# Kernel optimization log

Measured on AMD Instinct MI355X. Metric: run time of the kernel, lower is better.

## Reference

```python
import jax, jax.numpy as jnp
import numpy as np

V, D, H, L, E, DH, K, PMAX = 50257, 128, 4, 4, 8, 512, 2, 256
B, T = 8, 256


def setup_inputs() -> dict:
    key = jax.random.key(0)
    ks = jax.random.split(key, 10)
    s = 0.02
    def n(k, shape):
        return jax.random.normal(k, shape, jnp.float32) * s
    return dict(
        idx=jax.random.randint(ks[0], (B, T), 0, V),
        tok_emb=n(ks[1], (V, D)),
        pos_emb=n(ks[2], (PMAX, D)),
        ln1_g=jnp.ones((L, D), jnp.float32), ln1_b=jnp.zeros((L, D), jnp.float32),
        in_w=n(ks[3], (L, 3 * D, D)), in_b=jnp.zeros((L, 3 * D), jnp.float32),
        out_w=n(ks[4], (L, D, D)), out_b=jnp.zeros((L, D), jnp.float32),
        ln2_g=jnp.ones((L, D), jnp.float32), ln2_b=jnp.zeros((L, D), jnp.float32),
        gate_w=n(ks[5], (L, E, D)),
        w1=n(ks[6], (L, E, DH, D)),
        w2=n(ks[7], (L, E, D, DH)),
        lnf_g=jnp.ones((D,), jnp.float32), lnf_b=jnp.zeros((D,), jnp.float32),
        lm_w=n(ks[8], (V, D)),
    )


def _ln(x, g, b):
    mu = x.mean(-1, keepdims=True)
    var = jnp.var(x, -1, keepdims=True)
    return (x - mu) / jnp.sqrt(var + 1e-5) * g + b


def _moe(x, gw, w1, w2):
    # x: [N, D]; top-2 sparse MoE, computed densely per expert then combined.
    logits = x @ gw.T                              # [N, E]
    probs = jax.nn.softmax(logits, -1)
    topw, topi = jax.lax.top_k(probs, K)           # [N, K]
    topw = topw / topw.sum(-1, keepdims=True)
    we = (topw[..., None] * jax.nn.one_hot(topi, E, dtype=x.dtype)).sum(1)  # [N, E]
    h = jax.nn.silu(jnp.einsum('nd,ehd->neh', x, w1))   # [N, E, DH]
    y = jnp.einsum('neh,edh->ned', h, w2)               # [N, E, D]
    return jnp.einsum('ned,ne->nd', y, we)


def reference(idx, tok_emb, pos_emb, ln1_g, ln1_b, in_w, in_b, out_w, out_b,
              ln2_g, ln2_b, gate_w, w1, w2, lnf_g, lnf_b, lm_w):
    b, t = idx.shape
    x = tok_emb[idx] + pos_emb[:t]                 # [B, T, D]
    dh = D // H
    scale = 1.0 / np.sqrt(dh)
    for l in range(L):
        xl = _ln(x, ln1_g[l], ln1_b[l])
        qkv = xl @ in_w[l].T + in_b[l]
        q, k, v = jnp.split(qkv, 3, -1)
        q = q.reshape(b, t, H, dh)
        k = k.reshape(b, t, H, dh)
        v = v.reshape(b, t, H, dh)
        att = jax.nn.softmax(jnp.einsum('bqhd,bkhd->bhqk', q, k) * scale, -1)
        o = jnp.einsum('bhqk,bkhd->bqhd', att, v).reshape(b, t, D)
        x = x + o @ out_w[l].T + out_b[l]
        x2 = _ln(x, ln2_g[l], ln2_b[l]).reshape(b * t, D)
        x = x + _moe(x2, gate_w[l], w1[l], w2[l]).reshape(b, t, D)
    return _ln(x, lnf_g, lnf_b) @ lm_w.T           # [B, T, V]
```

## Files before the change

### kernel.cpp

```cpp
#include <hip/hip_runtime.h>
#include <math.h>

#define NTOK 2048
#define DD   128
#define NHEAD 4
#define DHEAD 32
#define NLAYER 4
#define NEXP 8
#define DHID 512
#define NVOCAB 50257
#define VPAD  50304
#define SEQ   256
#define NBATCH 8

typedef __attribute__((ext_vector_type(8))) short short8v;
typedef __attribute__((ext_vector_type(4))) float f32x4;

__device__ __forceinline__ unsigned short nm_bf16r(float f) {
  unsigned u = __float_as_uint(f);
  u += 0x7fffu + ((u >> 16) & 1u);
  return (unsigned short)(u >> 16);
}

__device__ __forceinline__ float nm_silu(float a) {
  return a / (1.f + __expf(-a));
}

template<int N4>
__device__ __forceinline__ float nm_dotv(const float* __restrict__ a,
                                         const float* __restrict__ w) {
  const float4* a4 = (const float4*)a;
  const float4* w4 = (const float4*)w;
  float sx = 0.f, sy = 0.f, sz = 0.f, sw = 0.f;
#pragma unroll 16
  for (int k = 0; k < N4; ++k) {
    float4 av = a4[k], wv = w4[k];
    sx = fmaf(av.x, wv.x, sx);
    sy = fmaf(av.y, wv.y, sy);
    sz = fmaf(av.z, wv.z, sz);
    sw = fmaf(av.w, wv.w, sw);
  }
  return (sx + sy) + (sz + sw);
}

#define C3_LMW 6438912ull
#define C3_W1  6963200ull
#define C3_ALL 7487488ull
#define CVTB   7312
__global__ __launch_bounds__(256) void nm_init(
    const int* __restrict__ idx, const float* __restrict__ tok,
    const float* __restrict__ pos, const float* __restrict__ g,
    const float* __restrict__ b, const float* __restrict__ lmw,
    const float* __restrict__ w1l3, const float* __restrict__ w2l3,
    float* __restrict__ x, float* __restrict__ xl,
    unsigned short* __restrict__ lmwb, unsigned short* __restrict__ w1b3,
    unsigned short* __restrict__ w2b3, int* __restrict__ zp) {
  int bid = blockIdx.x, tid = threadIdx.x;
  if (bid < CVTB) {
    size_t base = ((size_t)bid * 256 + tid) * 4;
    if (base < (size_t)NVOCAB * DD) {
      float4 v = *(const float4*)(lmw + base);
      ushort4 us = {nm_bf16r(v.x), nm_bf16r(v.y), nm_bf16r(v.z), nm_bf16r(v.w)};
      *(ushort4*)(lmwb + base) = us;
    } else if (base < C3_LMW) {
      ushort4 us = {0, 0, 0, 0};
      *(ushort4*)(lmwb + base) = us;
    } else if (base < C3_W1) {
      size_t j = base - C3_LMW;
      float4 v = *(const float4*)(w1l3 + j);
      ushort4 us = {nm_bf16r(v.x), nm_bf16r(v.y), nm_bf16r(v.z), nm_bf16r(v.w)};
      *(ushort4*)(w1b3 + j) = us;
    } else {
      size_t j = base - C3_W1;
      float4 v = *(const float4*)(w2l3 + j);
      ushort4 us = {nm_bf16r(v.x), nm_bf16r(v.y), nm_bf16r(v.z), nm_bf16r(v.w)};
      *(ushort4*)(w2b3 + j) = us;
    }
  } else if (bid < CVTB + NTOK / 4) {
    int n = (bid - CVTB) * 4 + (tid >> 6);
    int lane = tid & 63;
    int t = idx[n];
    float v0 = tok[(size_t)t * DD + lane]      + pos[(n % SEQ) * DD + lane];
    float v1 = tok[(size_t)t * DD + lane + 64] + pos[(n % SEQ) * DD + lane + 64];
    x[n * DD + lane]      = v0;
    x[n * DD + lane + 64] = v1;
    float s = v0 + v1;
#pragma unroll
    for (int o = 32; o > 0; o >>= 1) s += __shfl_xor(s, o, 64);
    float mu = s * (1.f / 128.f);
    float d0 = v0 - mu, d1 = v1 - mu;
    float q = d0 * d0 + d1 * d1;
#pragma unroll
    for (int o = 32; o > 0; o >>= 1) q += __shfl_xor(q, o, 64);
    float rstd = rsqrtf(q * (1.f / 128.f) + 1e-5f);
    xl[n * DD + lane]      = d0 * rstd * g[lane]      + b[lane];
    xl[n * DD + lane + 64] = d1 * rstd * g[lane + 64] + b[lane + 64];
  } else {
    if (tid < 68) zp[tid] = 0;
  }
}

__global__ void nm_embed_ln(const int* __restrict__ idx, const float* __restrict__ tok,
                            const float* __restrict__ pos, const float* __restrict__ g,
                            const float* __restrict__ b, float* __restrict__ x,
                            float* __restrict__ xlf) {
  int n = blockIdx.x, lane = threadIdx.x;
  int t = idx[n];
  float v0 = tok[(size_t)t * DD + lane]      + pos[(n % SEQ) * DD + lane];
  float v1 = tok[(size_t)t * DD + lane + 64] + pos[(n % SEQ) * DD + lane + 64];
  x[n * DD + lane]      = v0;
  x[n * DD + lane + 64] = v1;
  float s = v0 + v1;
#pragma unroll
  for (int o = 32; o > 0; o >>= 1) s += __shfl_xor(s, o, 64);
  float mu = s * (1.f / 128.f);
  float d0 = v0 - mu, d1 = v1 - mu;
  float q = d0 * d0 + d1 * d1;
#pragma unroll
  for (int o = 32; o > 0; o >>= 1) q += __shfl_xor(q, o, 64);
  float rstd = rsqrtf(q * (1.f / 128.f) + 1e-5f);
  xlf[n * DD + lane]      = d0 * rstd * g[lane]      + b[lane];
  xlf[n * DD + lane + 64] = d1 * rstd * g[lane + 64] + b[lane + 64];
}

__global__ void nm_ln(const float* __restrict__ in, const float* __restrict__ g,
                      const float* __restrict__ b, float* __restrict__ out) {
  int n = blockIdx.x, lane = threadIdx.x;
  float v0 = in[n * DD + lane], v1 = in[n * DD + lane + 64];
  float s = v0 + v1;
#pragma unroll
  for (int o = 32; o > 0; o >>= 1) s += __shfl_xor(s, o, 64);
  float mu = s * (1.f / 128.f);
  float d0 = v0 - mu, d1 = v1 - mu;
  float q = d0 * d0 + d1 * d1;
#pragma unroll
  for (int o = 32; o > 0; o >>= 1) q += __shfl_xor(q, o, 64);
  float rstd = rsqrtf(q * (1.f / 128.f) + 1e-5f);
  out[n * DD + lane]      = d0 * rstd * g[lane]      + b[lane];
  out[n * DD + lane + 64] = d1 * rstd * g[lane + 64] + b[lane + 64];
}

__global__ void nm_combine_ln(const float* __restrict__ yb, const int* __restrict__ posm,
                              const float* __restrict__ topw, float* __restrict__ x,
                              const float* __restrict__ g, const float* __restrict__ b,
                              float* __restrict__ xl, unsigned short* __restrict__ xb) {
  int n = blockIdx.x, lane = threadIdx.x;
  float w0 = topw[2 * n], w1 = topw[2 * n + 1];
  int p0 = posm[2 * n], p1 = posm[2 * n + 1];
  float v0 = x[n * DD + lane]      + w0 * yb[(size_t)p0 * DD + lane]
                                   + w1 * yb[(size_t)p1 * DD + lane];
  float v1 = x[n * DD + lane + 64] + w0 * yb[(size_t)p0 * DD + lane + 64]
                                   + w1 * yb[(size_t)p1 * DD + lane + 64];
  x[n * DD + lane]      = v0;
  x[n * DD + lane + 64] = v1;
  float s = v0 + v1;
#pragma unroll
  for (int o = 32; o > 0; o >>= 1) s += __shfl_xor(s, o, 64);
  float mu = s * (1.f / 128.f);
  float d0 = v0 - mu, d1 = v1 - mu;
  float q = d0 * d0 + d1 * d1;
#pragma unroll
  for (int o = 32; o > 0; o >>= 1) q += __shfl_xor(q, o, 64);
  float rstd = rsqrtf(q * (1.f / 128.f) + 1e-5f);
  float o0 = d0 * rstd * g[lane]      + b[lane];
  float o1 = d1 * rstd * g[lane + 64] + b[lane + 64];
  xl[n * DD + lane]      = o0;
  xl[n * DD + lane + 64] = o1;
  if (xb) {
    xb[n * DD + lane]      = nm_bf16r(o0);
    xb[n * DD + lane + 64] = nm_bf16r(o1);
  }
}

template<int F, int MT>
__global__ __launch_bounds__(256) void nm_gemm2(
    const float* __restrict__ A, const float* __restrict__ B,
    float* __restrict__ C, const float* __restrict__ bias,
    int M, int N, int K,
    const int* __restrict__ list, const int* __restrict__ cnt,
    const int* __restrict__ off) {
  constexpr bool GA = F & 1, SI = F & 2, BI = F & 4, GR = F & 16;
  constexpr int RG = MT / 64;
  __shared__ __align__(16) float As[64][MT + 4];
  __shared__ __align__(16) float Bs[64][68];
  int tid = threadIdx.x;
  int n0 = blockIdx.x * 64, m0 = blockIdx.y * MT;
  int Mloc = M, o = 0;
  const float* Bb = B;
  if constexpr (GR) {
    int e = blockIdx.z;
    Mloc = cnt[e];
    if (m0 >= Mloc) return;
    o = off[e];
    Bb = B + (size_t)e * (size_t)N * K;
  }
  int tm = tid & 15, tn = tid >> 4;
  float acc[RG * 4][4] = {};
  for (int kc = 0; kc < K; kc += 64) {
#pragma unroll
    for (int i = 0; i < RG * 4; ++i) {
      int f = tid + 256 * i;
      int r = f >> 4, c4 = f & 15;
      int mi = m0 + r;
      if (mi >= Mloc) mi = m0;
      const float* ar;
      if constexpr (GA) ar = A + (size_t)(list[o + mi] >> 1) * K;
      else              ar = A + (size_t)(o + mi) * K;
      float4 v = *(const float4*)(ar + kc + c4 * 4);
      int k = c4 * 4;
      As[k][r] = v.x; As[k + 1][r] = v.y; As[k + 2][r] = v.z; As[k + 3][r] = v.w;
    }
#pragma unroll
    for (int i = 0; i < 4; ++i) {
      int f = tid + 256 * i;
      int r = f >> 4, c4 = f & 15;
      const float* br = Bb + (size_t)(n0 + r) * K + kc + c4 * 4;
      float4 v = *(const float4*)br;
      int k = c4 * 4;
      Bs[k][r] = v.x; Bs[k + 1][r] = v.y; Bs[k + 2][r] = v.z; Bs[k + 3][r] = v.w;
    }
    __syncthreads();
#pragma unroll 16
    for (int k = 0; k < 64; ++k) {
      float4 b = *(const float4*)&Bs[k][tn * 4];
#pragma unroll
      for (int g2 = 0; g2 < RG; ++g2) {
        float4 a = *(const float4*)&As[k][g2 * 64 + tm * 4];
        acc[g2*4+0][0] = fmaf(a.x, b.x, acc[g2*4+0][0]);
        acc[g2*4+0][1] = fmaf(a.x, b.y, acc[g2*4+0][1]);
        acc[g2*4+0][2] = fmaf(a.x, b.z, acc[g2*4+0][2]);
        acc[g2*4+0][3] = fmaf(a.x, b.w, acc[g2*4+0][3]);
        acc[g2*4+1][0] = fmaf(a.y, b.x, acc[g2*4+1][0]);
        acc[g2*4+1][1] = fmaf(a.y, b.y, acc[g2*4+1][1]);
        acc[g2*4+1][2] = fmaf(a.y, b.z, acc[g2*4+1][2]);
        acc[g2*4+1][3] = fmaf(a.y, b.w, acc[g2*4+1][3]);
        acc[g2*4+2][0] = fmaf(a.z, b.x, acc[g2*4+2][0]);
        acc[g2*4+2][1] = fmaf(a.z, b.y, acc[g2*4+2][1]);
        acc[g2*4+2][2] = fmaf(a.z, b.z, acc[g2*4+2][2]);
        acc[g2*4+2][3] = fmaf(a.z, b.w, acc[g2*4+2][3]);
        acc[g2*4+3][0] = fmaf(a.w, b.x, acc[g2*4+3][0]);
        acc[g2*4+3][1] = fmaf(a.w, b.y, acc[g2*4+3][1]);
        acc[g2*4+3][2] = fmaf(a.w, b.z, acc[g2*4+3][2]);
        acc[g2*4+3][3] = fmaf(a.w, b.w, acc[g2*4+3][3]);
      }
    }
    __syncthreads();
  }
  float4 bv = {0.f, 0.f, 0.f, 0.f};
  if constexpr (BI) bv = *(const float4*)(bias + n0 + tn * 4);
#pragma unroll
  for (int g2 = 0; g2 < RG; ++g2) {
#pragma unroll
    for (int i = 0; i < 4; ++i) {
      int row = m0 + g2 * 64 + tm * 4 + i;
      if (GR && row >= Mloc) continue;
      float* cr = C + (size_t)(o + row) * N + n0 + tn * 4;
      float r0 = acc[g2 * 4 + i][0], r1 = acc[g2 * 4 + i][1];
      float r2 = acc[g2 * 4 + i][2], r3 = acc[g2 * 4 + i][3];
      if constexpr (BI) { r0 += bv.x; r1 += bv.y; r2 += bv.z; r3 += bv.w; }
      if constexpr (SI) { r0 = nm_silu(r0); r1 = nm_silu(r1); r2 = nm_silu(r2); r3 = nm_silu(r3); }
      float4 st = {r0, r1, r2, r3};
      *(float4*)cr = st;
    }
  }
}

template<int F, int KK>
__global__ __launch_bounds__(256) void nm_bgemm(
    const unsigned short* __restrict__ A, const unsigned short* __restrict__ B,
    float* __restrict__ Cf, unsigned short* __restrict__ Cb,
    const float* __restrict__ bias, int M, int N,
    const int* __restrict__ list, const int* __restrict__ cnt,
    const int* __restrict__ off) {
  constexpr bool GA = F & 1, SI = F & 2, BI = F & 4, SB = F & 8, GR = F & 16;
  int wave = threadIdx.x >> 6, lane = threadIdx.x & 63;
  int n0 = blockIdx.x * 32;
  int m0 = blockIdx.y * 128 + wave * 32;
  int Mloc = M, o = 0;
  const unsigned short* Bb = B;
  if constexpr (GR) {
    int e = blockIdx.z;
    Mloc = cnt[e];
    o = off[e];
    Bb = B + (size_t)e * (size_t)N * KK;
  }
  if (m0 >= Mloc) return;
  int lr = lane & 15, lk = (lane >> 4) * 8;
  const unsigned short* arow[2];
#pragma unroll
  for (int i = 0; i < 2; ++i) {
    int mi = m0 + i * 16 + lr;
    if (mi >= Mloc) mi = Mloc - 1;
    int r = GA ? (list[o + mi] >> 1) : (o + mi);
    arow[i] = A + (size_t)r * KK;
  }
  const unsigned short* brow[2] = { Bb + (size_t)(n0 + lr) * KK,
                                    Bb + (size_t)(n0 + 16 + lr) * KK };
  f32x4 acc[2][2] = {};
#pragma unroll
  for (int ks = 0; ks < KK / 32; ++ks) {
    int kb = ks * 32 + lk;
    short8v a0 = *(const short8v*)(arow[0] + kb);
    short8v a1 = *(const short8v*)(arow[1] + kb);
    short8v b0 = *(const short8v*)(brow[0] + kb);
    short8v b1 = *(const short8v*)(brow[1] + kb);
    acc[0][0] = __builtin_amdgcn_mfma_f32_16x16x32_bf16(a0, b0, acc[0][0], 0, 0, 0);
    acc[0][1] = __builtin_amdgcn_mfma_f32_16x16x32_bf16(a0, b1, acc[0][1], 0, 0, 0);
    acc[1][0] = __builtin_amdgcn_mfma_f32_16x16x32_bf16(a1, b0, acc[1][0], 0, 0, 0);
    acc[1][1] = __builtin_amdgcn_mfma_f32_16x16x32_bf16(a1, b1, acc[1][1], 0, 0, 0);
  }
  float bc[2] = {0.f, 0.f};
  if constexpr (BI) {
    bc[0] = bias[n0 + (lane & 15)];
    bc[1] = bias[n0 + 16 + (lane & 15)];
  }
#pragma unroll
  for (int i = 0; i < 2; ++i) {
    int rbase = m0 + i * 16 + (lane >> 4) * 4;
#pragma unroll
    for (int r = 0; r < 4; ++r) {
      int row = rbase + r;
      if (GR && row >= Mloc) continue;
#pragma unroll
      for (int j = 0; j < 2; ++j) {
        float v = acc[i][j][r];
        if constexpr (BI) v += bc[j];
        if constexpr (SI) v = nm_silu(v);
        int col = n0 + j * 16 + (lane & 15);
        if constexpr (SB) Cb[(size_t)(o + row) * N + col] = nm_bf16r(v);
        else              Cf[(size_t)(o + row) * N + col] = v;
      }
    }
  }
}

__global__ __launch_bounds__(256) void nm_oplng(
    const float* __restrict__ ao, const float* __restrict__ w,
    const float* __restrict__ bias, float* __restrict__ x,
    const float* __restrict__ g, const float* __restrict__ b,
    float* __restrict__ xlf, unsigned short* __restrict__ xlb,
    const float* __restrict__ gw,
    int* __restrict__ topi, float* __restrict__ topw, int* __restrict__ cnt,
    int* __restrict__ ticket, int* __restrict__ off, int* __restrict__ list,
    int* __restrict__ posm) {
  __shared__ __align__(16) float As[64][36];
  __shared__ __align__(16) float Bs[64][132];
  __shared__ float Ls[32][9];
  __shared__ int doR;
  __shared__ int cv[NEXP], lcur[NEXP];
  int tid = threadIdx.x;
  int m0 = blockIdx.x * 32;
  int tm = tid >> 5, tn = tid & 31;
  float acc[4][4] = {};
  for (int kc = 0; kc < DD; kc += 64) {
#pragma unroll
    for (int i = 0; i < 2; ++i) {
      int ch = tid + 256 * i, r = ch >> 4, c4 = ch & 15;
      float4 v = *(const float4*)(ao + (size_t)(m0 + r) * DD + kc + c4 * 4);
      int k = c4 * 4;
      As[k][r] = v.x; As[k + 1][r] = v.y; As[k + 2][r] = v.z; As[k + 3][r] = v.w;
    }
#pragma unroll
    for (int i = 0; i < 8; ++i) {
      int ch = tid + 256 * i, r = ch >> 4, c4 = ch & 15;
      float4 v = *(const float4*)(w + (size_t)r * DD + kc + c4 * 4);
      int k = c4 * 4;
      Bs[k][r] = v.x; Bs[k + 1][r] = v.y; Bs[k + 2][r] = v.z; Bs[k + 3][r] = v.w;
    }
    __syncthreads();
#pragma unroll 8
    for (int k = 0; k < 64; ++k) {
      float4 a = *(const float4*)&As[k][tm * 4];
      float4 bb = *(const float4*)&Bs[k][tn * 4];
      acc[0][0] = fmaf(a.x, bb.x, acc[0][0]); acc[0][1] = fmaf(a.x, bb.y, acc[0][1]);
      acc[0][2] = fmaf(a.x, bb.z, acc[0][2]); acc[0][3] = fmaf(a.x, bb.w, acc[0][3]);
      acc[1][0] = fmaf(a.y, bb.x, acc[1][0]); acc[1][1] = fmaf(a.y, bb.y, acc[1][1]);
      acc[1][2] = fmaf(a.y, bb.z, acc[1][2]); acc[1][3] = fmaf(a.y, bb.w, acc[1][3]);
      acc[2][0] = fmaf(a.z, bb.x, acc[2][0]); acc[2][1] = fmaf(a.z, bb.y, acc[2][1]);
      acc[2][2] = fmaf(a.z, bb.z, acc[2][2]); acc[2][3] = fmaf(a.z, bb.w, acc[2][3]);
      acc[3][0] = fmaf(a.w, bb.x, acc[3][0]); acc[3][1] = fmaf(a.w, bb.y, acc[3][1]);
      acc[3][2] = fmaf(a.w, bb.z, acc[3][2]); acc[3][3] = fmaf(a.w, bb.w, acc[3][3]);
    }
    __syncthreads();
  }
  float4 bv = *(const float4*)(bias + tn * 4);
  float rr[4][4], s1[4], s2[4];
#pragma unroll
  for (int i = 0; i < 4; ++i) {
    int rw = m0 + tm * 4 + i;
    float4 xv = *(const float4*)(x + (size_t)rw * DD + tn * 4);
    float r0 = acc[i][0] + bv.x + xv.x;
    float r1 = acc[i][1] + bv.y + xv.y;
    float r2 = acc[i][2] + bv.z + xv.z;
    float r3 = acc[i][3] + bv.w + xv.w;
    rr[i][0] = r0; rr[i][1] = r1; rr[i][2] = r2; rr[i][3] = r3;
    float4 st = {r0, r1, r2, r3};
    *(float4*)(x + (size_t)rw * DD + tn * 4) = st;
    s1[i] = r0 + r1 + r2 + r3;
    s2[i] = r0 * r0 + r1 * r1 + r2 * r2 + r3 * r3;
  }
#pragma unroll
  for (int o = 16; o >= 1; o >>= 1) {
#pragma unroll
    for (int i = 0; i < 4; ++i) {
      s1[i] += __shfl_xor(s1[i], o, 64);
      s2[i] += __shfl_xor(s2[i], o, 64);
    }
  }
  float4 gv  = *(const float4*)(g + tn * 4);
  float4 bbv = *(const float4*)(b + tn * 4);
#pragma unroll
  for (int i = 0; i < 4; ++i) {
    int rw = m0 + tm * 4 + i;
    float mu = s1[i] * (1.f / 128.f);
    float var = s2[i] * (1.f / 128.f) - mu * mu;
    float rstd = rsqrtf(var + 1e-5f);
    float y0 = (rr[i][0] - mu) * rstd * gv.x + bbv.x;
    float y1 = (rr[i][1] - mu) * rstd * gv.y + bbv.y;
    float y2 = (rr[i][2] - mu) * rstd * gv.z + bbv.z;
    float y3 = (rr[i][3] - mu) * rstd * gv.w + bbv.w;
    float4 yv = {y0, y1, y2, y3};
    if (xlf) *(float4*)(xlf + (size_t)rw * DD + tn * 4) = yv;
    if (xlb) {
      ushort4 us = {nm_bf16r(y0), nm_bf16r(y1), nm_bf16r(y2), nm_bf16r(y3)};
      *(ushort4*)(xlb + (size_t)rw * DD + tn * 4) = us;
    }
    *(float4*)&Bs[tm * 4 + i][tn * 4] = yv;
  }
  __syncthreads();
  int grow = tid >> 3, ge = tid & 7;
  const float4* xr = (const float4*)&Bs[grow][0];
  const float4* wr = (const float4*)(gw + (size_t)ge * DD);
  float sx = 0.f, sy = 0.f, sz = 0.f, sw = 0.f;
#pragma unroll
  for (int k2 = 0; k2 < 32; ++k2) {
    float4 a = xr[k2], w4 = wr[k2];
    sx = fmaf(a.x, w4.x, sx); sy = fmaf(a.y, w4.y, sy);
    sz = fmaf(a.z, w4.z, sz); sw = fmaf(a.w, w4.w, sw);
  }
  Ls[grow][ge] = (sx + sy) + (sz + sw);
  __syncthreads();
  if (ge == 0) {
    float gl[NEXP];
#pragma unroll
    for (int e = 0; e < NEXP; ++e) gl[e] = Ls[grow][e];
    int i0 = 0;
#pragma unroll
    for (int e = 1; e < NEXP; ++e) if (gl[e] > gl[i0]) i0 = e;
    int i1 = (i0 == 0) ? 1 : 0;
#pragma unroll
    for (int e = 0; e < NEXP; ++e) { if (e != i0 && gl[e] > gl[i1]) i1 = e; }
    float p1 = __expf(gl[i1] - gl[i0]);
    float inv = 1.f / (1.f + p1);
    int n = m0 + grow;
    topi[2 * n] = i0; topi[2 * n + 1] = i1;
    topw[2 * n] = inv; topw[2 * n + 1] = p1 * inv;
    atomicAdd(cnt + i0, 1);
    atomicAdd(cnt + i1, 1);
  }
  __syncthreads();
  if (tid == 0) {
    __threadfence();
    doR = (atomicAdd(ticket, 1) == 63);
    if (doR) __threadfence();
  }
  __syncthreads();
  if (doR) {
    if (tid < NEXP) cv[tid] = atomicAdd(cnt + tid, 0);
    __syncthreads();
    if (tid < NEXP) {
      int o2 = 0;
      for (int e = 0; e < tid; ++e) o2 += cv[e];
      lcur[tid] = o2;
      off[tid] = o2;
    }
    __syncthreads();
    for (int t = tid; t < 2 * NTOK; t += 256) {
      int e = topi[t];
      int p = atomicAdd(&lcur[e], 1);
      list[p] = t;
      posm[t] = p;
    }
  }
}

__global__ __launch_bounds__(256) void nm_attn2(const float* __restrict__ qkv,
                                                float* __restrict__ o) {
  __shared__ __align__(16) float Ks[SEQ][DHEAD];
  __shared__ __align__(16) float Vs[SEQ][DHEAD];
  __shared__ float mbuf[32][9], sbuf[32][9];
  __shared__ __align__(16) float accbuf[32][36];
  int bh = blockIdx.x;
  int b = bh >> 2, h = bh & 3;
  int qt = blockIdx.y;
  int tid = threadIdx.x;
  const float* base = qkv + (size_t)b * SEQ * 384;
  for (int f = tid; f < SEQ * 8; f += 256) {
    int t = f >> 3, c4 = f & 7;
    float4 kv = *(const float4*)(base + (size_t)t * 384 + 128 + h * DHEAD + c4 * 4);
    float4 vv = *(const float4*)(base + (size_t)t * 384 + 256 + h * DHEAD + c4 * 4);
    *(float4*)&Ks[t][c4 * 4] = kv;
    *(float4*)&Vs[t][c4 * 4] = vv;
  }
  __syncthreads();
  int q = tid & 31, slot = tid >> 5;
  int tq = qt * 32 + q;
  float qv[DHEAD];
  const float4* q4 = (const float4*)(base + (size_t)tq * 384 + h * DHEAD);
#pragma unroll
  for (int k = 0; k < 8; ++k) {
    float4 v = q4[k];
    qv[4*k] = v.x; qv[4*k+1] = v.y; qv[4*k+2] = v.z; qv[4*k+3] = v.w;
  }
  float m = -1e30f, s = 0.f, acc[DHEAD];
#pragma unroll
  for (int d = 0; d < DHEAD; ++d) acc[d] = 0.f;
  const float scale = 0.17677669529663687f;
  int j0 = slot * 32;
  for (int jj = 0; jj < 32; ++jj) {
    int j = j0 + jj;
    const float4* kr = (const float4*)Ks[j];
    float sc = 0.f;
#pragma unroll
    for (int k = 0; k < 8; ++k) {
      float4 v = kr[k];
      sc += qv[4*k]*v.x + qv[4*k+1]*v.y + qv[4*k+2]*v.z + qv[4*k+3]*v.w;
    }
    sc *= scale;
    float mn = fmaxf(m, sc);
    float f = __expf(m - mn), p = __expf(sc - mn);
    s = s * f + p;
    const float4* vr = (const float4*)Vs[j];
#pragma unroll
    for (int k = 0; k < 8; ++k) {
      float4 v = vr[k];
      acc[4*k]   = acc[4*k]  * f + p * v.x;
      acc[4*k+1] = acc[4*k+1]* f + p * v.y;
      acc[4*k+2] = acc[4*k+2]* f + p * v.z;
      acc[4*k+3] = acc[4*k+3]* f + p * v.w;
    }
    m = mn;
  }
  mbuf[q][slot] = m;
  sbuf[q][slot] = s;
  __syncthreads();
  float M = mbuf[q][0];
#pragma unroll
  for (int t = 1; t < 8; ++t) M = fmaxf(M, mbuf[q][t]);
  float S = 0.f;
#pragma unroll
  for (int t = 0; t < 8; ++t) S += sbuf[q][t] * __expf(mbuf[q][t] - M);
  float w = __expf(m - M);
#pragma unroll
  for (int d = 0; d < DHEAD; ++d) acc[d] *= w;
#pragma unroll
  for (int p = 0; p < 8; ++p) {
    if (slot == p) {
      if (p == 0) {
#pragma unroll
        for (int d = 0; d < DHEAD; ++d) accbuf[q][d] = acc[d];
      } else {
#pragma unroll
        for (int d = 0; d < DHEAD; ++d) accbuf[q][d] += acc[d];
      }
    }
    __syncthreads();
  }
  if (slot == 0) sbuf[q][8] = 1.f / S;
  __syncthreads();
  int q2 = tid >> 3, c4 = tid & 7;
  float inv = sbuf[q2][8];
  float4 v = *(const float4*)&accbuf[q2][c4 * 4];
  v.x *= inv; v.y *= inv; v.z *= inv; v.w *= inv;
  *(float4*)(o + (size_t)(b * SEQ + qt * 32 + q2) * DD + h * DHEAD + c4 * 4) = v;
}

__global__ void nm_qkv(const float* __restrict__ xl, const float* __restrict__ w,
                       const float* __restrict__ bias, float* __restrict__ qkv) {
  __shared__ __align__(16) float xs[DD];
  int n = blockIdx.x, tid = threadIdx.x;
  xs[tid] = xl[n * DD + tid];
  __syncthreads();
#pragma unroll
  for (int jj = 0; jj < 3; ++jj) {
    int j = tid + jj * 128;
    qkv[(size_t)n * 384 + j] = nm_dotv<32>(xs, w + (size_t)j * DD) + bias[j];
  }
}

__global__ void nm_outproj(const float* __restrict__ ao, const float* __restrict__ w,
                           const float* __restrict__ bias, float* __restrict__ x) {
  __shared__ __align__(16) float os[DD];
  int n = blockIdx.x, tid = threadIdx.x;
  os[tid] = ao[n * DD + tid];
  __syncthreads();
  x[n * DD + tid] += nm_dotv<32>(os, w + (size_t)tid * DD) + bias[tid];
}

__global__ void nm_moe(const float* __restrict__ x2, const float* __restrict__ gw,
                       const float* __restrict__ w1, const float* __restrict__ w2,
                       float* __restrict__ x) {
  __shared__ __align__(16) float xs[DD];
  __shared__ __align__(16) float hs[DHID];
  __shared__ float gl[NEXP];
  __shared__ int   ei[2];
  __shared__ float ew[2];
  int n = blockIdx.x, tid = threadIdx.x;
  if (tid < DD) xs[tid] = x2[n * DD + tid];
  __syncthreads();
  if (tid < NEXP) gl[tid] = nm_dotv<32>(xs, gw + (size_t)tid * DD);
  __syncthreads();
  if (tid == 0) {
    int i0 = 0;
#pragma unroll
    for (int e = 1; e < NEXP; ++e) if (gl[e] > gl[i0]) i0 = e;
    int i1 = (i0 == 0) ? 1 : 0;
    for (int e = 0; e < NEXP; ++e) { if (e == i0) continue; if (gl[e] > gl[i1]) i1 = e; }
    float p1 = __expf(gl[i1] - gl[i0]);
    float inv = 1.f / (1.f + p1);
    ei[0] = i0; ei[1] = i1; ew[0] = inv; ew[1] = p1 * inv;
  }
  __syncthreads();
  float yacc = 0.f;
  for (int t2 = 0; t2 < 2; ++t2) {
    int e = ei[t2];
    float wt = ew[t2];
    const float* w1e = w1 + (size_t)e * DHID * DD;
#pragma unroll
    for (int jj = 0; jj < 2; ++jj) {
      int j = tid + jj * 256;
      float a = nm_dotv<32>(xs, w1e + (size_t)j * DD);
      hs[j] = nm_silu(a);
    }
    __syncthreads();
    if (tid < DD) yacc += wt * nm_dotv<128>(hs, w2 + ((size_t)e * DD + tid) * DHID);
    __syncthreads();
  }
  if (tid < DD) x[n * DD + tid] += yacc;
}

__device__ __forceinline__ short8v nm_cvt8(const float* p) {
  const float4* p4 = (const float4*)p;
  float4 a = p4[0], b = p4[1];
  short8v r;
  r[0] = (short)nm_bf16r(a.x); r[1] = (short)nm_bf16r(a.y);
  r[2] = (short)nm_bf16r(a.z); r[3] = (short)nm_bf16r(a.w);
  r[4] = (short)nm_bf16r(b.x); r[5] = (short)nm_bf16r(b.y);
  r[6] = (short)nm_bf16r(b.z); r[7] = (short)nm_bf16r(b.w);
  return r;
}

__global__ __launch_bounds__(256) void nm_lmhead_f32(
    const float* __restrict__ xf, const float* __restrict__ lmw,
    float* __restrict__ out) {
  int wave = threadIdx.x >> 6, lane = threadIdx.x & 63;
  int wr = wave >> 1, wc = wave & 1;
  int row0 = blockIdx.y * 128 + wr * 64;
  int col0 = blockIdx.x * 128 + wc * 64;
  int lr = lane & 15, lk = (lane >> 4) * 8;
  f32x4 acc[4][4] = {};
#pragma unroll
  for (int ks = 0; ks < 4; ++ks) {
    int kb = ks * 32 + lk;
    short8v a[4], b[4];
#pragma unroll
    for (int i = 0; i < 4; ++i)
      a[i] = nm_cvt8(xf + (size_t)(row0 + i * 16 + lr) * DD + kb);
#pragma unroll
    for (int j = 0; j < 4; ++j) {
      int c = col0 + j * 16 + lr;
      if (c < NVOCAB) b[j] = nm_cvt8(lmw + (size_t)c * DD + kb);
      else {
        short8v z;
#pragma unroll
        for (int e = 0; e < 8; ++e) z[e] = 0;
        b[j] = z;
      }
    }
#pragma unroll
    for (int i = 0; i < 4; ++i)
#pragma unroll
      for (int j = 0; j < 4; ++j)
        acc[i][j] = __builtin_amdgcn_mfma_f32_16x16x32_bf16(a[i], b[j], acc[i][j], 0, 0, 0);
  }
  int cr = (lane >> 4) * 4;
#pragma unroll
  for (int j = 0; j < 4; ++j) {
    int c = col0 + j * 16 + (lane & 15);
    if (c < NVOCAB) {
#pragma unroll
      for (int i = 0; i < 4; ++i)
#pragma unroll
        for (int r = 0; r < 4; ++r)
          out[(size_t)(row0 + i * 16 + cr + r) * NVOCAB + c] = acc[i][j][r];
    }
  }
}

__global__ __launch_bounds__(256) void nm_lmhead2(
    const unsigned short* __restrict__ xfb, const unsigned short* __restrict__ lmwb,
    float* __restrict__ out) {
  __shared__ __align__(16) unsigned char smem[132 * 128 * 4];
  unsigned short* Ab = (unsigned short*)smem;
  unsigned short* Bb = Ab + 128 * 128;
  int tid = threadIdx.x;
  int row0 = blockIdx.y * 128, col0 = blockIdx.x * 128;
#pragma unroll
  for (int i = 0; i < 8; ++i) {
    int ch = tid + i * 256;
    int r = ch >> 4, s = ch & 15;
    int sg = s ^ (r & 7);
    *(short8v*)&Ab[r * 128 + s * 8] =
        *(const short8v*)(xfb + (size_t)(row0 + r) * DD + sg * 8);
    *(short8v*)&Bb[r * 128 + s * 8] =
        *(const short8v*)(lmwb + (size_t)(col0 + r) * DD + sg * 8);
  }
  __syncthreads();
  int wave = tid >> 6, lane = tid & 63;
  int wr = wave >> 1, wc = wave & 1;
  int lr = lane & 15, hk = lane >> 4;
  f32x4 acc[4][4] = {};
#pragma unroll
  for (int ks = 0; ks < 4; ++ks) {
    int sg = ks * 4 + hk;
    int sx = (sg ^ (lr & 7)) * 8;
    short8v a[4], b[4];
#pragma unroll
    for (int i = 0; i < 4; ++i)
      a[i] = *(const short8v*)&Ab[(wr * 64 + i * 16 + lr) * 128 + sx];
#pragma unroll
    for (int j = 0; j < 4; ++j)
      b[j] = *(const short8v*)&Bb[(wc * 64 + j * 16 + lr) * 128 + sx];
#pragma unroll
    for (int i = 0; i < 4; ++i)
#pragma unroll
      for (int j = 0; j < 4; ++j)
        acc[i][j] = __builtin_amdgcn_mfma_f32_16x16x32_bf16(a[i], b[j], acc[i][j], 0, 0, 0);
  }
  __syncthreads();
  float* Cs = (float*)smem;
  int hi4 = hk * 4;
#pragma unroll
  for (int j = 0; j < 4; ++j)
#pragma unroll
    for (int i = 0; i < 4; ++i)
#pragma unroll
      for (int r = 0; r < 4; ++r)
        Cs[(wr * 64 + i * 16 + hi4 + r) * 132 + wc * 64 + j * 16 + lr] = acc[i][j][r];
  __syncthreads();
  bool full = (col0 + 128 <= NVOCAB);
#pragma unroll 4
  for (int rr = 0; rr < 32; ++rr) {
    int row = wave * 32 + rr;
    float v0 = Cs[row * 132 + lane];
    float v1 = Cs[row * 132 + 64 + lane];
    size_t base = (size_t)(row0 + row) * NVOCAB + col0;
    if (full) {
      out[base + lane] = v0;
      out[base + 64 + lane] = v1;
    } else {
      if (col0 + lane < NVOCAB)      out[base + lane] = v0;
      if (col0 + 64 + lane < NVOCAB) out[base + 64 + lane] = v1;
    }
  }
}

extern "C" void kernel_launch(void* const* d_in, const int* in_sizes, int n_in,
                              void* d_out, int out_size, void* d_ws, size_t ws_size,
                              hipStream_t stream) {
  const int*   idx   = (const int*)  d_in[0];
  const float* tok   = (const float*)d_in[1];
  const float* pos   = (const float*)d_in[2];
  const float* ln1g  = (const float*)d_in[3];
  const float* ln1b  = (const float*)d_in[4];
  const float* inw   = (const float*)d_in[5];
  const float* inb   = (const float*)d_in[6];
  const float* outw  = (const float*)d_in[7];
  const float* outb  = (const float*)d_in[8];
  const float* ln2g  = (const float*)d_in[9];
  const float* ln2b  = (const float*)d_in[10];
  const float* gatew = (const float*)d_in[11];
  const float* w1    = (const float*)d_in[12];
  const float* w2    = (const float*)d_in[13];
  const float* lnfg  = (const float*)d_in[14];
  const float* lnfb  = (const float*)d_in[15];
  const float* lmw   = (const float*)d_in[16];
  float* out = (float*)d_out;

  float* ws   = (float*)d_ws;
  float* x    = ws;
  float* xl   = x    + NTOK * DD;
  float* qkv  = xl   + NTOK * DD;
  float* ao   = qkv  + NTOK * 384;
  float* topw = ao   + NTOK * DD;
  float* H    = topw + 2 * NTOK;
  float* yb   = H    + 2 * NTOK * DHID;
  int*   topi = (int*)(yb + 2 * NTOK * DD);
  int*   list = topi + 2 * NTOK;
  int*   posm = list + 2 * NTOK;
  int*   cnt  = posm + 2 * NTOK;
  int*   offs = cnt  + NLAYER * NEXP;
  int*   tick = offs + NLAYER * NEXP;
  unsigned short* xlb  = (unsigned short*)(tick + 8);
  unsigned short* Hb   = xlb + NTOK * DD;
  unsigned short* xfb  = Hb  + 2 * NTOK * DHID;
  unsigned short* w1b3 = xfb + NTOK * DD;
  unsigned short* w2b3 = w1b3 + NEXP * DHID * DD;
  unsigned short* lmwb = w2b3 + NEXP * DD * DHID;
  const size_t need = (size_t)((char*)(lmwb + (size_t)VPAD * DD) - (char*)d_ws);
  const bool pre = (ws_size >= need);

  const float* w1l3 = w1 + (size_t)3 * NEXP * DHID * DD;
  const float* w2l3 = w2 + (size_t)3 * NEXP * DD * DHID;

  if (pre) {
    nm_init<<<CVTB + NTOK / 4 + 1, 256, 0, stream>>>(
        idx, tok, pos, ln1g, ln1b, lmw, w1l3, w2l3, x, xl, lmwb, w1b3, w2b3, cnt);
    for (int l = 0; l < NLAYER; ++l) {
      nm_gemm2<4, 128><<<dim3(384 / 64, NTOK / 128), 256, 0, stream>>>(
          xl, inw + (size_t)l * 384 * DD, qkv, inb + (size_t)l * 384,
          NTOK, 384, DD, nullptr, nullptr, nullptr);
      nm_attn2<<<dim3(NBATCH * NHEAD, SEQ / 32), 256, 0, stream>>>(qkv, ao);
      nm_oplng<<<NTOK / 32, 256, 0, stream>>>(
          ao, outw + (size_t)l * DD * DD, outb + (size_t)l * DD, x,
          ln2g + l * DD, ln2b + l * DD, xl, (l == 3) ? xlb : (unsigned short*)nullptr,
          gatew + (size_t)l * NEXP * DD, topi, topw, cnt + l * NEXP,
          tick + l, offs + l * NEXP, list, posm);
      int* cnt_l = cnt + l * NEXP;
      int* off_l = offs + l * NEXP;
      if (l < 3) {
        const float* w1l = w1 + (size_t)l * NEXP * DHID * DD;
        const float* w2l = w2 + (size_t)l * NEXP * DD * DHID;
        nm_gemm2<19, 128><<<dim3(DHID / 64, 2 * NTOK / 128, NEXP), 256, 0, stream>>>(
            xl, w1l, H, nullptr, 0, DHID, DD, list, cnt_l, off_l);
        nm_gemm2<16, 64><<<dim3(DD / 64, 2 * NTOK / 64, NEXP), 256, 0, stream>>>(
            H, w2l, yb, nullptr, 0, DD, DHID, nullptr, cnt_l, off_l);
      } else {
        nm_bgemm<27, 128><<<dim3(DHID / 32, 32, NEXP), 256, 0, stream>>>(
            xlb, w1b3, nullptr, Hb, nullptr, 0, DHID, list, cnt_l, off_l);
        nm_bgemm<16, 512><<<dim3(DD / 32, 32, NEXP), 256, 0, stream>>>(
            Hb, w2b3, yb, nullptr, nullptr, 0, DD, nullptr, cnt_l, off_l);
      }
      const float* gN = (l < NLAYER - 1) ? ln1g + (l + 1) * DD : lnfg;
      const float* bN = (l < NLAYER - 1) ? ln1b + (l + 1) * DD : lnfb;
      nm_combine_ln<<<NTOK, 64, 0, stream>>>(
          yb, posm, topw, x, gN, bN, xl,
          (l == NLAYER - 1) ? xfb : (unsigned short*)nullptr);
    }
    nm_lmhead2<<<dim3(VPAD / 128, NTOK / 128), 256, 0, stream>>>(xfb, lmwb, out);
  } else {
    nm_embed_ln<<<NTOK, 64, 0, stream>>>(idx, tok, pos, ln1g, ln1b, x, xl);
    for (int l = 0; l < NLAYER; ++l) {
      nm_qkv<<<NTOK, 128, 0, stream>>>(xl, inw + (size_t)l * 384 * DD,
                                       inb + (size_t)l * 384, qkv);
      nm_attn2<<<dim3(NBATCH * NHEAD, SEQ / 32), 256, 0, stream>>>(qkv, ao);
      nm_outproj<<<NTOK, 128, 0, stream>>>(ao, outw + (size_t)l * DD * DD,
                                           outb + (size_t)l * DD, x);
      nm_ln<<<NTOK, 64, 0, stream>>>(x, ln2g + l * DD, ln2b + l * DD, xl);
      nm_moe<<<NTOK, 256, 0, stream>>>(xl, gatew + (size_t)l * NEXP * DD,
                                       w1 + (size_t)l * NEXP * DHID * DD,
                                       w2 + (size_t)l * NEXP * DD * DHID, x);
      const float* gN = (l < NLAYER - 1) ? ln1g + (l + 1) * DD : lnfg;
      const float* bN = (l < NLAYER - 1) ? ln1b + (l + 1) * DD : lnfb;
      nm_ln<<<NTOK, 64, 0, stream>>>(x, gN, bN, xl);
    }
    nm_lmhead_f32<<<dim3(VPAD / 128, NTOK / 128), 256, 0, stream>>>(xl, lmw, out);
  }
}
```

Baseline: 828.4 us.

## Restructure attention to 16 queries per block with swizzled shared K/V

Replaces the attention kernel with a version that processes 16 queries per block, each split across 16 key slots, stores K/V in shared memory with an XOR-style rotation to avoid bank conflicts, and merges partial softmax states in one pass instead of a serialized 8-step accumulation with repeated barriers. The grid doubles along the query dimension, which increases parallelism at the cost of reloading K/V twice as often. QKV and first MoE GEMM tile heights are also halved to launch more blocks, and the oplng kernel now always writes the fp32 LN output.

```diff
diff --git a/kernel.cpp b/kernel.cpp
--- a/kernel.cpp
+++ b/kernel.cpp
@@ -96,7 +96,7 @@
     xl[n * DD + lane]      = d0 * rstd * g[lane]      + b[lane];
     xl[n * DD + lane + 64] = d1 * rstd * g[lane + 64] + b[lane + 64];
   } else {
-    if (tid < 68) zp[tid] = 0;
+    if (tid < 72) zp[tid] = 0;
   }
 }
 
@@ -338,7 +338,7 @@
     const float* __restrict__ ao, const float* __restrict__ w,
     const float* __restrict__ bias, float* __restrict__ x,
     const float* __restrict__ g, const float* __restrict__ b,
-    float* __restrict__ xlf, unsigned short* __restrict__ xlb,
+    float* __restrict__ xl, unsigned short* __restrict__ xlb,
     const float* __restrict__ gw,
     int* __restrict__ topi, float* __restrict__ topw, int* __restrict__ cnt,
     int* __restrict__ ticket, int* __restrict__ off, int* __restrict__ list,
@@ -420,7 +420,7 @@
     float y2 = (rr[i][2] - mu) * rstd * gv.z + bbv.z;
     float y3 = (rr[i][3] - mu) * rstd * gv.w + bbv.w;
     float4 yv = {y0, y1, y2, y3};
-    if (xlf) *(float4*)(xlf + (size_t)rw * DD + tn * 4) = yv;
+    *(float4*)(xl + (size_t)rw * DD + tn * 4) = yv;
     if (xlb) {
       ushort4 us = {nm_bf16r(y0), nm_bf16r(y1), nm_bf16r(y2), nm_bf16r(y3)};
       *(ushort4*)(xlb + (size_t)rw * DD + tn * 4) = us;
@@ -484,12 +484,11 @@
   }
 }
 
-__global__ __launch_bounds__(256) void nm_attn2(const float* __restrict__ qkv,
+__global__ __launch_bounds__(256) void nm_attn3(const float* __restrict__ qkv,
                                                 float* __restrict__ o) {
-  __shared__ __align__(16) float Ks[SEQ][DHEAD];
-  __shared__ __align__(16) float Vs[SEQ][DHEAD];
-  __shared__ float mbuf[32][9], sbuf[32][9];
-  __shared__ __align__(16) float accbuf[32][36];
+  __shared__ __align__(16) float smem[2 * SEQ * DHEAD];
+  float4* K4 = (float4*)smem;
+  float4* V4 = (float4*)(smem + SEQ * DHEAD);
   int bh = blockIdx.x;
   int b = bh >> 2, h = bh & 3;
   int qt = blockIdx.y;
@@ -497,14 +496,13 @@
   const float* base = qkv + (size_t)b * SEQ * 384;
   for (int f = tid; f < SEQ * 8; f += 256) {
     int t = f >> 3, c4 = f & 7;
-    float4 kv = *(const float4*)(base + (size_t)t * 384 + 128 + h * DHEAD + c4 * 4);
-    float4 vv = *(const float4*)(base + (size_t)t * 384 + 256 + h * DHEAD + c4 * 4);
-    *(float4*)&Ks[t][c4 * 4] = kv;
-    *(float4*)&Vs[t][c4 * 4] = vv;
-  }
-  __syncthreads();
-  int q = tid & 31, slot = tid >> 5;
-  int tq = qt * 32 + q;
+    int pc = (c4 + (t >> 4)) & 7;
+    K4[t * 8 + pc] = *(const float4*)(base + (size_t)t * 384 + 128 + h * DHEAD + c4 * 4);
+    V4[t * 8 + pc] = *(const float4*)(base + (size_t)t * 384 + 256 + h * DHEAD + c4 * 4);
+  }
+  __syncthreads();
+  int qi = tid >> 4, slot = tid & 15;
+  int tq = qt * 16 + qi;
   float qv[DHEAD];
   const float4* q4 = (const float4*)(base + (size_t)tq * 384 + h * DHEAD);
 #pragma unroll
@@ -516,24 +514,22 @@
 #pragma unroll
   for (int d = 0; d < DHEAD; ++d) acc[d] = 0.f;
   const float scale = 0.17677669529663687f;
-  int j0 = slot * 32;
-  for (int jj = 0; jj < 32; ++jj) {
-    int j = j0 + jj;
-    const float4* kr = (const float4*)Ks[j];
+  int sw = slot & 7;
+  for (int jj = 0; jj < 16; ++jj) {
+    int j = slot * 16 + jj;
     float sc = 0.f;
 #pragma unroll
     for (int k = 0; k < 8; ++k) {
-      float4 v = kr[k];
+      float4 v = K4[j * 8 + ((k + sw) & 7)];
       sc += qv[4*k]*v.x + qv[4*k+1]*v.y + qv[4*k+2]*v.z + qv[4*k+3]*v.w;
     }
     sc *= scale;
     float mn = fmaxf(m, sc);
     float f = __expf(m - mn), p = __expf(sc - mn);
     s = s * f + p;
-    const float4* vr = (const float4*)Vs[j];
 #pragma unroll
     for (int k = 0; k < 8; ++k) {
-      float4 v = vr[k];
+      float4 v = V4[j * 8 + ((k + sw) & 7)];
       acc[4*k]   = acc[4*k]  * f + p * v.x;
       acc[4*k+1] = acc[4*k+1]* f + p * v.y;
       acc[4*k+2] = acc[4*k+2]* f + p * v.z;
@@ -541,38 +537,31 @@
     }
     m = mn;
   }
-  mbuf[q][slot] = m;
-  sbuf[q][slot] = s;
-  __syncthreads();
-  float M = mbuf[q][0];
-#pragma unroll
-  for (int t = 1; t < 8; ++t) M = fmaxf(M, mbuf[q][t]);
-  float S = 0.f;
-#pragma unroll
-  for (int t = 0; t < 8; ++t) S += sbuf[q][t] * __expf(mbuf[q][t] - M);
-  float w = __expf(m - M);
-#pragma unroll
-  for (int d = 0; d < DHEAD; ++d) acc[d] *= w;
-#pragma unroll
-  for (int p = 0; p < 8; ++p) {
-    if (slot == p) {
-      if (p == 0) {
-#pragma unroll
-        for (int d = 0; d < DHEAD; ++d) accbuf[q][d] = acc[d];
-      } else {
-#pragma unroll
-        for (int d = 0; d < DHEAD; ++d) accbuf[q][d] += acc[d];
-      }
-    }
-    __syncthreads();
-  }
-  if (slot == 0) sbuf[q][8] = 1.f / S;
-  __syncthreads();
-  int q2 = tid >> 3, c4 = tid & 7;
-  float inv = sbuf[q2][8];
-  float4 v = *(const float4*)&accbuf[q2][c4 * 4];
-  v.x *= inv; v.y *= inv; v.z *= inv; v.w *= inv;
-  *(float4*)(o + (size_t)(b * SEQ + qt * 32 + q2) * DD + h * DHEAD + c4 * 4) = v;
+  __syncthreads();
+  float* cb = smem;
+  float* my = cb + (qi * 16 + slot) * 34;
+#pragma unroll
+  for (int d = 0; d < DHEAD; ++d) my[d] = acc[d];
+  my[32] = m;
+  my[33] = s;
+  __syncthreads();
+  int q2 = tid >> 4, dg = tid & 15;
+  const float* qb = cb + q2 * 16 * 34;
+  float M = qb[32];
+#pragma unroll
+  for (int t = 1; t < 16; ++t) M = fmaxf(M, qb[t * 34 + 32]);
+  float S = 0.f, v0 = 0.f, v1 = 0.f;
+#pragma unroll
+  for (int t = 0; t < 16; ++t) {
+    float w = __expf(qb[t * 34 + 32] - M);
+    S += qb[t * 34 + 33] * w;
+    v0 += w * qb[t * 34 + dg * 2];
+    v1 += w * qb[t * 34 + dg * 2 + 1];
+  }
+  float inv = 1.f / S;
+  float* orow = o + (size_t)(b * SEQ + qt * 16 + q2) * DD + h * DHEAD + dg * 2;
+  orow[0] = v0 * inv;
+  orow[1] = v1 * inv;
 }
 
 __global__ void nm_qkv(const float* __restrict__ xl, const float* __restrict__ w,
@@ -817,10 +806,10 @@
     nm_init<<<CVTB + NTOK / 4 + 1, 256, 0, stream>>>(
         idx, tok, pos, ln1g, ln1b, lmw, w1l3, w2l3, x, xl, lmwb, w1b3, w2b3, cnt);
     for (int l = 0; l < NLAYER; ++l) {
-      nm_gemm2<4, 128><<<dim3(384 / 64, NTOK / 128), 256, 0, stream>>>(
+      nm_gemm2<4, 64><<<dim3(384 / 64, NTOK / 64), 256, 0, stream>>>(
           xl, inw + (size_t)l * 384 * DD, qkv, inb + (size_t)l * 384,
           NTOK, 384, DD, nullptr, nullptr, nullptr);
-      nm_attn2<<<dim3(NBATCH * NHEAD, SEQ / 32), 256, 0, stream>>>(qkv, ao);
+      nm_attn3<<<dim3(NBATCH * NHEAD, SEQ / 16), 256, 0, stream>>>(qkv, ao);
       nm_oplng<<<NTOK / 32, 256, 0, stream>>>(
           ao, outw + (size_t)l * DD * DD, outb + (size_t)l * DD, x,
           ln2g + l * DD, ln2b + l * DD, xl, (l == 3) ? xlb : (unsigned short*)nullptr,
@@ -831,7 +820,7 @@
       if (l < 3) {
         const float* w1l = w1 + (size_t)l * NEXP * DHID * DD;
         const float* w2l = w2 + (size_t)l * NEXP * DD * DHID;
-        nm_gemm2<19, 128><<<dim3(DHID / 64, 2 * NTOK / 128, NEXP), 256, 0, stream>>>(
+        nm_gemm2<19, 64><<<dim3(DHID / 64, 2 * NTOK / 64, NEXP), 256, 0, stream>>>(
             xl, w1l, H, nullptr, 0, DHID, DD, list, cnt_l, off_l);
         nm_gemm2<16, 64><<<dim3(DD / 64, 2 * NTOK / 64, NEXP), 256, 0, stream>>>(
             H, w2l, yb, nullptr, 0, DD, DHID, nullptr, cnt_l, off_l);
@@ -853,7 +842,7 @@
     for (int l = 0; l < NLAYER; ++l) {
       nm_qkv<<<NTOK, 128, 0, stream>>>(xl, inw + (size_t)l * 384 * DD,
                                        inb + (size_t)l * 384, qkv);
-      nm_attn2<<<dim3(NBATCH * NHEAD, SEQ / 32), 256, 0, stream>>>(qkv, ao);
+      nm_attn3<<<dim3(NBATCH * NHEAD, SEQ / 16), 256, 0, stream>>>(qkv, ao);
       nm_outproj<<<NTOK, 128, 0, stream>>>(ao, outw + (size_t)l * DD * DD,
                                            outb + (size_t)l * DD, x);
       nm_ln<<<NTOK, 64, 0, stream>>>(x, ln2g + l * DD, ln2b + l * DD, xl);
```

After: 766.9 us. 7.4% less time.
